# Kernel optimization log

Hardware: AMD Instinct MI355X
Metric: run time of the kernel (lower is better)

## Reference

```python
import jax, jax.numpy as jnp
import numpy as np

S = 4096
D_MODEL = 1024
D_INTERNAL = 4096


def setup_inputs() -> dict:
    key = jax.random.key(0)
    ks = jax.random.split(key, 12)
    s = 0.02
    return {
        "x": jax.random.normal(ks[0], (S, D_MODEL), dtype=jnp.float32),
        # projection weights stored as [d_in, d_out] so y = x @ W + b
        "Wq": jax.random.normal(ks[1], (D_MODEL, D_MODEL), dtype=jnp.float32) * s,
        "bq": jnp.zeros((D_MODEL,), dtype=jnp.float32),
        "Wk": jax.random.normal(ks[2], (D_MODEL, D_MODEL), dtype=jnp.float32) * s,
        "bk": jnp.zeros((D_MODEL,), dtype=jnp.float32),
        "Wv": jax.random.normal(ks[3], (D_MODEL, D_MODEL), dtype=jnp.float32) * s,
        "bv": jnp.zeros((D_MODEL,), dtype=jnp.float32),
        "W1": jax.random.normal(ks[4], (D_MODEL, D_INTERNAL), dtype=jnp.float32) * s,
        "b1": jnp.zeros((D_INTERNAL,), dtype=jnp.float32),
        "W2": jax.random.normal(ks[5], (D_INTERNAL, D_MODEL), dtype=jnp.float32) * s,
        "b2": jnp.zeros((D_MODEL,), dtype=jnp.float32),
    }


def reference(x, Wq, bq, Wk, bk, Wv, bv, W1, b1, W2, b2):
    # x: [S, D] (module is unbatched: k.transpose(0,1) implies 2-D input)
    d_model = x.shape[-1]
    q = x @ Wq + bq                         # [S, D]
    k = x @ Wk + bk                         # [S, D]
    v = x @ Wv + bv                         # [S, D]
    scores = (q @ k.T) / jnp.sqrt(jnp.asarray(d_model, x.dtype))  # [S, S]
    s = x.shape[0]
    causal = jnp.triu(jnp.ones((s, s), dtype=bool), k=1)           # True above diag
    scores = jnp.where(causal, jnp.asarray(-1e9, x.dtype), scores)
    attn = jax.nn.softmax(scores, axis=-1)  # [S, S]
    attended = attn @ v                     # [S, D]
    h = x + attended                        # residual 1
    ff = jax.nn.relu(h @ W1 + b1) @ W2 + b2 # 2-layer MLP
    out = h + ff                            # residual 2
    return (out, attn)
```

## Files before the change

### kernel.cpp

```cpp
#include <hip/hip_runtime.h>
#include <hip/hip_bf16.h>


typedef __attribute__((ext_vector_type(4))) float  f32x4;
typedef __attribute__((ext_vector_type(8))) short  bf16x8;
typedef __attribute__((ext_vector_type(4))) unsigned short us4;
typedef __attribute__((ext_vector_type(8))) unsigned short us8;

#define DEVINL __device__ __forceinline__

static constexpr int S   = 4096;
static constexpr int DM  = 1024;
static constexpr int DI  = 4096;

DEVINL unsigned short f2bf(float f) {
  union { float f; unsigned u; } v; v.f = f;
  unsigned r = v.u + 0x7fffu + ((v.u >> 16) & 1u);
  return (unsigned short)(r >> 16);
}

DEVINL float bf2f(unsigned short b) {
  union { unsigned u; float f; } v; v.u = ((unsigned)b) << 16;
  return v.f;
}

DEVINL void gld_lds16(const unsigned short* g, unsigned short* l) {
  __builtin_amdgcn_global_load_lds(
      (const __attribute__((address_space(1))) void*)g,
      (__attribute__((address_space(3))) void*)l,
      16, 0, 0);
}

DEVINL int xcd_remap(int orig, int nwg) {
  const int q = nwg >> 3, r = nwg & 7;
  const int x = orig & 7, idx = orig >> 3;
  return (x < r ? x * (q + 1) : r * (q + 1) + (x - r) * q) + idx;
}

__global__ void prep_all(const float* __restrict__ x,
                         const float* __restrict__ Wq,
                         const float* __restrict__ Wk,
                         const float* __restrict__ Wv,
                         const float* __restrict__ W1,
                         const float* __restrict__ W2,
                         const float* __restrict__ bq,
                         const float* __restrict__ bk,
                         const float* __restrict__ bv,
                         unsigned short* __restrict__ xb,
                         unsigned short* __restrict__ Wqkvt,
                         unsigned short* __restrict__ W1t,
                         unsigned short* __restrict__ W2t,
                         float* __restrict__ bqkv) {
  __shared__ float tile[32][33];
  const int b = blockIdx.x;
  const int tid = threadIdx.x;

  if (b < 2048) {
    long i = ((long)b * 256 + tid) * 8;
    f32x4 a = *(const f32x4*)(x + i);
    f32x4 c = *(const f32x4*)(x + i + 4);
    us8 o;
    o[0] = f2bf(a[0]); o[1] = f2bf(a[1]); o[2] = f2bf(a[2]); o[3] = f2bf(a[3]);
    o[4] = f2bf(c[0]); o[5] = f2bf(c[1]); o[6] = f2bf(c[2]); o[7] = f2bf(c[3]);
    *(us8*)(xb + i) = o;
    return;
  }
  if (b >= 13312) {
    const int t = b - 13312;
    const float* src = (t == 0) ? bq : (t == 1) ? bk : bv;
    const int i = tid * 4;
    *(f32x4*)(bqkv + t * DM + i) = *(const f32x4*)(src + i);
    return;
  }

  const float* in; unsigned short* out; int R, C, t;
  if (b < 3072)      { in = Wq; out = Wqkvt;                      R = DM; C = DM; t = b - 2048; }
  else if (b < 4096) { in = Wk; out = Wqkvt + (size_t)DM * DM;    R = DM; C = DM; t = b - 3072; }
  else if (b < 5120) { in = Wv; out = Wqkvt + 2 * (size_t)DM * DM;R = DM; C = DM; t = b - 4096; }
  else if (b < 9216) { in = W1; out = W1t;                        R = DM; C = DI; t = b - 5120; }
  else               { in = W2; out = W2t;                        R = DI; C = DM; t = b - 9216; }
  const int gx = C >> 5;
  const int bx = (t % gx) * 32, by = (t / gx) * 32;
  const int tx = tid & 31, ty = tid >> 5;
  #pragma unroll
  for (int j = 0; j < 4; ++j) {
    int r = ty + j * 8;
    tile[r][tx] = in[(size_t)(by + r) * C + bx + tx];
  }
  __syncthreads();
  #pragma unroll
  for (int j = 0; j < 4; ++j) {
    int r = ty + j * 8;
    out[(size_t)(bx + r) * R + by + tx] = f2bf(tile[tx][r]);
  }
}

__global__ void transpose_bf16(const unsigned short* __restrict__ in, int ld,
                               unsigned short* __restrict__ out, int ldo) {
  __shared__ unsigned short tile[32][33];
  const int bx = blockIdx.x * 32, by = blockIdx.y * 32;
  const int tx = threadIdx.x, ty = threadIdx.y;
  #pragma unroll
  for (int j = 0; j < 4; ++j) {
    int r = ty + j * 8;
    tile[r][tx] = in[(size_t)(by + r) * ld + bx + tx];
  }
  __syncthreads();
  #pragma unroll
  for (int j = 0; j < 4; ++j) {
    int r = ty + j * 8;
    out[(size_t)(bx + r) * ldo + by + tx] = tile[tx][r];
  }
}

enum { EPI_QKV = 0, EPI_SCE = 1, EPI_FF1 = 4, EPI_PART = 6 };

#define VM_WAIT0 asm volatile("s_waitcnt vmcnt(0)" ::: "memory")

template <int EPI, bool TRI_PACK, bool TRI_TRUNC>
__launch_bounds__(256, 3)
__global__ void gemm4(const unsigned short* __restrict__ A,
                      const unsigned short* __restrict__ Bt,
                      int M, int N, int K, int lda, int ldb, int kChunk, int GX,
                      const float* __restrict__ bias,
                      float* __restrict__ Cf,
                      unsigned short* __restrict__ Cb,
                      float scale) {
  const int wg = xcd_remap(blockIdx.x, gridDim.x);
  int bm, bn;
  if (TRI_PACK) {
    int t = wg;
    bm = (int)((sqrtf(8.f * (float)t + 1.f) - 1.f) * 0.5f);
    while ((bm + 1) * (bm + 2) / 2 <= t) ++bm;
    while (bm * (bm + 1) / 2 > t) --bm;
    bn = t - bm * (bm + 1) / 2;
  } else {
    const int GY_ = gridDim.x / GX;
    const int bpp = GY_ * 8;
    const int panel = wg / bpp, rem = wg % bpp;
    bm = rem >> 3;
    bn = panel * 8 + (rem & 7);
  }
  const int bm0 = bm * 128, bn0 = bn * 128;

  const int kbeg = blockIdx.z * kChunk;
  int kend = min(K, kbeg + kChunk);
  if (TRI_TRUNC) kend = min(kend, bm0 + 128);
  const int len = kend - kbeg;
  const int NT = (len > 0) ? (len >> 5) : 0;

  __shared__ __align__(16) unsigned short lds[2 * 8192];

  const int tid  = threadIdx.x;
  const int lane = tid & 63;
  const int w    = tid >> 6;
  const int wr   = w >> 1, wc = w & 1;
  const int fr   = lane & 15, fq = lane >> 4;

  f32x4 acc[4][4] = {};

  const int tq = tid >> 2;
  const int swcolE = ((tid & 3) * 8) ^ ((tq & 6) << 2);
  const unsigned short* gA = A  + (size_t)(bm0 + tq) * lda + kbeg + swcolE;
  const unsigned short* gB = Bt + (size_t)(bn0 + tq) * ldb + kbeg + swcolE;
  const size_t aH = (size_t)64 * lda, bH = (size_t)64 * ldb;

  auto stage = [&](int buf, int t_) {
    unsigned short* base = (unsigned short*)lds + buf * 8192;
    const size_t go = (size_t)t_ * 32;
    gld_lds16(gA + go,      base + w * 512);
    gld_lds16(gA + aH + go, base + 2048 + w * 512);
    gld_lds16(gB + go,      base + 4096 + w * 512);
    gld_lds16(gB + bH + go, base + 6144 + w * 512);
  };

  const int frSw = (fq * 8) ^ ((fr & 6) << 2);
  auto rdA = [&](int buf, int mi) {
    return *(const bf16x8*)((const unsigned short*)lds + buf * 8192 +
                            (wr * 64 + mi * 16 + fr) * 32 + frSw);
  };
  auto rdB = [&](int buf, int ni) {
    return *(const bf16x8*)((const unsigned short*)lds + buf * 8192 + 4096 +
                            (wc * 64 + ni * 16 + fr) * 32 + frSw);
  };

  if (NT > 0) {
    stage(0, 0);
    VM_WAIT0;
    __builtin_amdgcn_s_barrier();

    for (int t = 0; t < NT; ++t) {
      const int cur = t & 1, nxt = cur ^ 1;
      const bool pf = (t + 1 < NT);
      if (pf) stage(nxt, t + 1);

      bf16x8 a[4], b[4];
      #pragma unroll
      for (int mi = 0; mi < 4; ++mi) a[mi] = rdA(cur, mi);
      #pragma unroll
      for (int ni = 0; ni < 4; ++ni) b[ni] = rdB(cur, ni);
      #pragma unroll
      for (int mi = 0; mi < 4; ++mi)
        #pragma unroll
        for (int ni = 0; ni < 4; ++ni)
          acc[mi][ni] = __builtin_amdgcn_mfma_f32_16x16x32_bf16(
              a[mi], b[ni], acc[mi][ni], 0, 0, 0);

      if (pf) { VM_WAIT0; }
      __builtin_amdgcn_s_barrier();
    }
  }

  const int row0 = bm0 + wr * 64 + fq * 4;
  const int col0 = bn0 + wc * 64 + fr;
  const size_t zoff = (EPI == EPI_PART) ? (size_t)blockIdx.z * M * N : 0;
  #pragma unroll
  for (int ni = 0; ni < 4; ++ni) {
    const int col = col0 + ni * 16;
    float bval = 0.f;
    if (EPI == EPI_QKV || EPI == EPI_FF1) bval = bias[col];
    #pragma unroll
    for (int mi = 0; mi < 4; ++mi) {
      #pragma unroll
      for (int j = 0; j < 4; ++j) {
        const int row = row0 + mi * 16 + j;
        const size_t idx = zoff + (size_t)row * N + col;
        const float c = acc[mi][ni][j];
        if (EPI == EPI_QKV) {
          Cb[idx] = f2bf(c + bval);
        } else if (EPI == EPI_SCE) {
          const float e = (col <= row) ? __expf(c * scale) : 0.f;
          Cb[idx] = f2bf(e);
        } else if (EPI == EPI_FF1) {
          const float r = c + bval;
          Cb[idx] = f2bf(r > 0.f ? r : 0.f);
        } else {
          Cf[idx] = c;
        }
      }
    }
  }
}

__global__ void normalize_rows(const unsigned short* __restrict__ attnb,
                               float* __restrict__ attnf,
                               float* __restrict__ rowsum) {
  const int m = blockIdx.x;
  const int tid = threadIdx.x;
  const int valid = m + 1;
  const unsigned short* rowb = attnb + (size_t)m * S;
  float* rowf = attnf + (size_t)m * S;

  float v[4][4];
  float lsum = 0.f;
  #pragma unroll
  for (int i = 0; i < 4; ++i) {
    const int idx = tid * 4 + i * 1024;
    #pragma unroll
    for (int j = 0; j < 4; ++j) v[i][j] = 0.f;
    if (i * 1024 <= m) {
      us4 b = *(const us4*)(rowb + idx);
      #pragma unroll
      for (int j = 0; j < 4; ++j) {
        const float e = (idx + j < valid) ? bf2f(b[j]) : 0.f;
        v[i][j] = e;
        lsum += e;
      }
    }
  }
  #pragma unroll
  for (int off = 32; off > 0; off >>= 1)
    lsum += __shfl_xor(lsum, off, 64);

  __shared__ float red[4];
  if ((tid & 63) == 0) red[tid >> 6] = lsum;
  __syncthreads();
  const float total = red[0] + red[1] + red[2] + red[3];
  if (tid == 0) rowsum[m] = total;
  const float inv = 1.0f / total;

  #pragma unroll
  for (int i = 0; i < 4; ++i) {
    const int idx = tid * 4 + i * 1024;
    f32x4 o;
    #pragma unroll
    for (int j = 0; j < 4; ++j) o[j] = v[i][j] * inv;
    *(f32x4*)(rowf + idx) = o;
  }
}

template <bool FINAL, bool NORM>
__global__ void reduce_k(const float* __restrict__ P,
                         const float* __restrict__ res,
                         const float* __restrict__ bias,
                         const float* __restrict__ rowsum,
                         float* __restrict__ outf,
                         unsigned short* __restrict__ outb, long n) {
  long i = ((long)blockIdx.x * 256 + threadIdx.x) * 4;
  if (i >= n) return;
  f32x4 a = *(const f32x4*)(P + i);
  f32x4 b = *(const f32x4*)(P + n + i);
  f32x4 r = *(const f32x4*)(res + i);
  float inv = 1.f;
  if (NORM) inv = 1.0f / rowsum[i >> 10];
  if (FINAL) {
    f32x4 bb = *(const f32x4*)(bias + (i & (DM - 1)));
    f32x4 o;
    #pragma unroll
    for (int j = 0; j < 4; ++j) o[j] = a[j] + b[j] + r[j] + bb[j];
    *(f32x4*)(outf + i) = o;
  } else {
    f32x4 o; us4 ob;
    #pragma unroll
    for (int j = 0; j < 4; ++j) {
      o[j] = (a[j] + b[j]) * inv + r[j];
      ob[j] = f2bf(o[j]);
    }
    *(f32x4*)(outf + i) = o;
    *(us4*)(outb + i) = ob;
  }
}

extern "C" void kernel_launch(void* const* d_in, const int* in_sizes, int n_in,
                              void* d_out, int out_size, void* d_ws, size_t ws_size,
                              hipStream_t stream) {
  const float* x  = (const float*)d_in[0];
  const float* Wq = (const float*)d_in[1];
  const float* bq = (const float*)d_in[2];
  const float* Wk = (const float*)d_in[3];
  const float* bk = (const float*)d_in[4];
  const float* Wv = (const float*)d_in[5];
  const float* bv = (const float*)d_in[6];
  const float* W1 = (const float*)d_in[7];
  const float* b1 = (const float*)d_in[8];
  const float* W2 = (const float*)d_in[9];
  const float* b2 = (const float*)d_in[10];
  (void)in_sizes; (void)n_in; (void)out_size; (void)ws_size;

  float* outp  = (float*)d_out;
  float* attnf = (float*)d_out + (size_t)S * DM;

  const size_t MB = 1ull << 20;
  char* ws = (char*)d_ws;
  unsigned short* W2t   = (unsigned short*)(ws + 0 * MB);
  unsigned short* W1t   = (unsigned short*)(ws + 8 * MB);
  float*          h     = (float*)(ws + 16 * MB);
  unsigned short* hb    = (unsigned short*)(ws + 32 * MB);
  unsigned short* vt    = (unsigned short*)(ws + 40 * MB);
  unsigned short* attnb = (unsigned short*)(ws + 48 * MB);
  unsigned short* qkv   = (unsigned short*)(ws + 80 * MB);
  unsigned short* xb    = (unsigned short*)(ws + 104 * MB);
  unsigned short* Wqkvt = (unsigned short*)(ws + 112 * MB);
  float*          bqkv  = (float*)(ws + 118 * MB);
  float*          rowsum= (float*)(ws + 119 * MB);
  unsigned short* ff1b  = (unsigned short*)(ws + 40 * MB);
  float*          Ppv   = (float*)(ws + 80 * MB);
  float*          Pff   = (float*)(ws + 72 * MB);

  prep_all<<<dim3(13315), 256, 0, stream>>>(
      x, Wq, Wk, Wv, W1, W2, bq, bk, bv, xb, Wqkvt, W1t, W2t, bqkv);

  gemm4<EPI_QKV, false, false><<<dim3((S / 128) * (3072 / 128), 1, 1), 256, 0, stream>>>(
      xb, Wqkvt, S, 3072, DM, DM, DM, DM, 3072 / 128, bqkv, nullptr, qkv, 1.f);
  transpose_bf16<<<dim3(DM / 32, S / 32), dim3(32, 8), 0, stream>>>(
      qkv + 2 * DM, 3072, vt, S);

  gemm4<EPI_SCE, true, false><<<dim3(528, 1, 1), 256, 0, stream>>>(
      qkv, qkv + DM, S, S, DM, 3072, 3072, DM, 0, nullptr, nullptr, attnb, 0.03125f);

  normalize_rows<<<dim3(S), 256, 0, stream>>>(attnb, attnf, rowsum);

  gemm4<EPI_PART, false, true><<<dim3((S / 128) * (DM / 128), 1, 2), 256, 0, stream>>>(
      attnb, vt, S, DM, S, S, S, S / 2, DM / 128, nullptr, Ppv, nullptr, 1.f);
  reduce_k<false, true><<<dim3((S * DM) / 1024), 256, 0, stream>>>(
      Ppv, x, nullptr, rowsum, h, hb, (long)S * DM);

  gemm4<EPI_FF1, false, false><<<dim3((S / 128) * (DI / 128), 1, 1), 256, 0, stream>>>(
      hb, W1t, S, DI, DM, DM, DM, DM, DI / 128, b1, nullptr, ff1b, 1.f);

  gemm4<EPI_PART, false, false><<<dim3((S / 128) * (DM / 128), 1, 2), 256, 0, stream>>>(
      ff1b, W2t, S, DM, DI, DI, DI, DI / 2, DM / 128, nullptr, Pff, nullptr, 1.f);
  reduce_k<true, false><<<dim3((S * DM) / 1024), 256, 0, stream>>>(
      Pff, h, b2, nullptr, outp, nullptr, (long)S * DM);
}
```

Baseline: 247.0 us.

## Give each wave private LDS tiles to remove block-wide barriers in GEMM

Result: slower. 336.7 us (+36.3%).

```diff
diff --git a/kernel.cpp b/kernel.cpp
--- a/kernel.cpp
+++ b/kernel.cpp
@@ -118,7 +118,7 @@
 #define VM_WAIT0 asm volatile("s_waitcnt vmcnt(0)" ::: "memory")
 
 template <int EPI, bool TRI_PACK, bool TRI_TRUNC>
-__launch_bounds__(256, 3)
+__launch_bounds__(256, 2)
 __global__ void gemm4(const unsigned short* __restrict__ A,
                       const unsigned short* __restrict__ Bt,
                       int M, int N, int K, int lda, int ldb, int kChunk, int GX,
@@ -149,7 +149,7 @@
   const int len = kend - kbeg;
   const int NT = (len > 0) ? (len >> 5) : 0;
 
-  __shared__ __align__(16) unsigned short lds[2 * 8192];
+  __shared__ __align__(16) unsigned short lds[4 * 2 * 4096];
 
   const int tid  = threadIdx.x;
   const int lane = tid & 63;
@@ -159,40 +159,39 @@
 
   f32x4 acc[4][4] = {};
 
-  const int tq = tid >> 2;
-  const int swcolE = ((tid & 3) * 8) ^ ((tq & 6) << 2);
-  const unsigned short* gA = A  + (size_t)(bm0 + tq) * lda + kbeg + swcolE;
-  const unsigned short* gB = Bt + (size_t)(bn0 + tq) * ldb + kbeg + swcolE;
-  const size_t aH = (size_t)64 * lda, bH = (size_t)64 * ldb;
-
-  auto stage = [&](int buf, int t_) {
-    unsigned short* base = (unsigned short*)lds + buf * 8192;
+  const int lrow   = lane >> 2;
+  const int swcolE = ((lane & 3) * 8) ^ ((lrow & 6) << 2);
+  const unsigned short* gAw = A  + (size_t)(bm0 + wr * 64 + lrow) * lda + kbeg + swcolE;
+  const unsigned short* gBw = Bt + (size_t)(bn0 + wc * 64 + lrow) * ldb + kbeg + swcolE;
+
+  auto stageW = [&](int buf, int t_) {
+    unsigned short* base = (unsigned short*)lds + w * 8192 + buf * 4096;
     const size_t go = (size_t)t_ * 32;
-    gld_lds16(gA + go,      base + w * 512);
-    gld_lds16(gA + aH + go, base + 2048 + w * 512);
-    gld_lds16(gB + go,      base + 4096 + w * 512);
-    gld_lds16(gB + bH + go, base + 6144 + w * 512);
+    #pragma unroll
+    for (int i = 0; i < 4; ++i) {
+      gld_lds16(gAw + (size_t)(i * 16) * lda + go, base + i * 512);
+      gld_lds16(gBw + (size_t)(i * 16) * ldb + go, base + 2048 + i * 512);
+    }
   };
 
   const int frSw = (fq * 8) ^ ((fr & 6) << 2);
   auto rdA = [&](int buf, int mi) {
-    return *(const bf16x8*)((const unsigned short*)lds + buf * 8192 +
-                            (wr * 64 + mi * 16 + fr) * 32 + frSw);
+    return *(const bf16x8*)((const unsigned short*)lds + w * 8192 + buf * 4096 +
+                            (mi * 16 + fr) * 32 + frSw);
   };
   auto rdB = [&](int buf, int ni) {
-    return *(const bf16x8*)((const unsigned short*)lds + buf * 8192 + 4096 +
-                            (wc * 64 + ni * 16 + fr) * 32 + frSw);
+    return *(const bf16x8*)((const unsigned short*)lds + w * 8192 + buf * 4096 +
+                            2048 + (ni * 16 + fr) * 32 + frSw);
   };
 
   if (NT > 0) {
-    stage(0, 0);
+    stageW(0, 0);
     VM_WAIT0;
-    __builtin_amdgcn_s_barrier();
 
     for (int t = 0; t < NT; ++t) {
-      const int cur = t & 1, nxt = cur ^ 1;
+      const int cur = t & 1;
       const bool pf = (t + 1 < NT);
-      if (pf) stage(nxt, t + 1);
+      if (pf) stageW(cur ^ 1, t + 1);
 
       bf16x8 a[4], b[4];
       #pragma unroll
@@ -207,7 +206,6 @@
               a[mi], b[ni], acc[mi][ni], 0, 0, 0);
 
       if (pf) { VM_WAIT0; }
-      __builtin_amdgcn_s_barrier();
     }
   }
 
```
